# Kernel optimization log

Measured on AMD Instinct MI355X. Metric: run time of the kernel, lower is better.

Reference implementation:

```python
import jax, jax.numpy as jnp
import numpy as np

K = 7      # kernel size per spatial dim (kernel=[7,7])
PAD = 3    # padding per side ('same' for stride 1)
COUT = 64  # output width of the per-patch linear func


def _unfold(x):
    """convPrep: pad + unfold into sliding-window patches.
    x: [B, H, W] -> patches [B, H, W, K*K] (im2col, zero 'constant' padding)."""
    p = jax.lax.conv_general_dilated_patches(
        x[:, None, :, :],                # [B, 1, H, W]
        filter_shape=(K, K),
        window_strides=(1, 1),
        padding=[(PAD, PAD), (PAD, PAD)])
    # p: [B, K*K, H, W] -> [B, H, W, K*K]
    return jnp.moveaxis(p, 1, -1)


def setup_inputs() -> dict:
    key = jax.random.key(0)
    k1, k2 = jax.random.split(key, 2)
    x = jax.random.normal(k1, (8, 384, 384), dtype=jnp.float32)
    W = jax.random.normal(k2, (K * K, COUT), dtype=jnp.float32) / np.sqrt(K * K).astype(np.float32)
    b = jnp.zeros((COUT,), dtype=jnp.float32)
    return {"x": x, "W": W, "b": b}


def reference(x, W, b):
    # convPrep (pad+unfold) -> func (linear per flattened patch) -> convPost (fold back)
    patches = _unfold(x)                               # [B, H, W, K*K]
    out = jnp.einsum('bhwk,kc->bhwc', patches, W) + b  # [B, H, W, COUT]
    return out
```

## Files before the change

### kernel.cpp

```cpp
#include <hip/hip_runtime.h>


#define HH 384
#define WWID 384
#define BB 8
#define COUTC 64
#define TPX 64
#define TILES_PER_ROW 6
#define NTILES (BB * HH * TILES_PER_ROW)
#define NBLOCKS 2048
#define TILES_PER_BLOCK (NTILES / NBLOCKS)

typedef __attribute__((ext_vector_type(8))) __bf16 bf16x8;
typedef __attribute__((ext_vector_type(4))) float f32x4;

__global__ __launch_bounds__(256)
void conv7_mfma(const float* __restrict__ xg, const float* __restrict__ wg,
                const float* __restrict__ bg, float* __restrict__ out)
{
    __shared__ __bf16 xt[10][72];
    const int tid  = threadIdx.x;
    const int lane = tid & 63;
    const int wv   = tid >> 6;
    const int lq   = lane >> 4;
    const int lr   = lane & 15;

    bf16x8 bfr[2][4];
#pragma unroll
    for (int ch = 0; ch < 2; ++ch)
#pragma unroll
        for (int g = 0; g < 4; ++g) {
            bf16x8 f;
#pragma unroll
            for (int j = 0; j < 8; ++j) {
                const int k = ch * 32 + lq * 8 + j;
                f[j] = (k < 49) ? (__bf16)wg[k * COUTC + g * 16 + lr] : (__bf16)0.f;
            }
            bfr[ch][g] = f;
        }
    float biasv[4];
#pragma unroll
    for (int g = 0; g < 4; ++g) biasv[g] = bg[g * 16 + lr];

    int aoffp[2][8];
#pragma unroll
    for (int ch = 0; ch < 2; ++ch)
#pragma unroll
        for (int j = 0; j < 8; ++j) {
            const int k  = ch * 32 + lq * 8 + j;
            const int ky = k / 7, kx = k - ky * 7;
            aoffp[ch][j] = ky * 72 + kx + wv * 16 + lr;
        }

    for (int i = tid; i < 3 * 72; i += 256)
        (&xt[0][0])[7 * 72 + i] = (__bf16)0.f;

    for (int it = 0; it < TILES_PER_BLOCK; ++it) {
        const int tile = blockIdx.x * TILES_PER_BLOCK + it;
        const int t  = tile % TILES_PER_ROW;
        const int rh = tile / TILES_PER_ROW;
        const int h  = rh % HH;
        const int b  = rh / HH;
        const int w0 = t * TPX;

        __syncthreads();
        for (int i = tid; i < 490; i += 256) {
            const int r  = i / 70;
            const int c  = i - r * 70;
            const int hs = h - 3 + r;
            const int ws = w0 - 3 + c;
            float v = 0.f;
            if (hs >= 0 && hs < HH && ws >= 0 && ws < WWID)
                v = xg[((size_t)b * HH + hs) * WWID + ws];
            xt[r][c] = (__bf16)v;
        }
        __syncthreads();

        bf16x8 af[2];
#pragma unroll
        for (int ch = 0; ch < 2; ++ch) {
            bf16x8 f;
#pragma unroll
            for (int j = 0; j < 8; ++j)
                f[j] = (&xt[0][0])[aoffp[ch][j]];
            af[ch] = f;
        }

        f32x4 acc[4];
#pragma unroll
        for (int g = 0; g < 4; ++g)
            acc[g] = (f32x4){biasv[g], biasv[g], biasv[g], biasv[g]};
#pragma unroll
        for (int ch = 0; ch < 2; ++ch)
#pragma unroll
            for (int g = 0; g < 4; ++g)
                acc[g] = __builtin_amdgcn_mfma_f32_16x16x32_bf16(
                    af[ch], bfr[ch][g], acc[g], 0, 0, 0);

        float* obase = out + (((size_t)b * HH + h) * WWID + w0 + wv * 16) * COUTC;
#pragma unroll
        for (int g = 0; g < 4; ++g)
#pragma unroll
            for (int rr = 0; rr < 4; ++rr)
                obase[(size_t)(lq * 4 + rr) * COUTC + g * 16 + lr] = acc[g][rr];
    }
}

extern "C" void kernel_launch(void* const* d_in, const int* in_sizes, int n_in,
                              void* d_out, int out_size, void* d_ws, size_t ws_size,
                              hipStream_t stream) {
    const float* x = (const float*)d_in[0];
    const float* w = (const float*)d_in[1];
    const float* b = (const float*)d_in[2];
    float* out = (float*)d_out;
    (void)in_sizes; (void)n_in; (void)out_size; (void)d_ws; (void)ws_size;
    conv7_mfma<<<NBLOCKS, 256, 0, stream>>>(x, w, b, out);
}
```

Measured before the change: 330.5 us.

## Drop LDS staging; load patches from global and swap MFMA operands for vector stores

Removes the shared-memory tile and block-wide barriers, so each wave independently loads its 7x8 input window directly from global memory into registers, with a fast interior path and a clamped border path. The K dimension is re-laid out as ky*8+kx with zero padding so each lane's fragment is a contiguous row segment. MFMA operands are swapped (weights as A, input as B), which lets each lane write four contiguous output channels as a single float4 store instead of scalar strided stores. The cost is redundant global loads across lanes and waves, which now rely on cache hits.

```diff
diff --git a/kernel.cpp b/kernel.cpp
--- a/kernel.cpp
+++ b/kernel.cpp
@@ -2,30 +2,31 @@
 
 
 #define HH 384
-#define WWID 384
+#define WW 384
 #define BB 8
-#define COUTC 64
-#define TPX 64
-#define TILES_PER_ROW 6
-#define NTILES (BB * HH * TILES_PER_ROW)
+#define CC 64
+#define TPW 16
+#define TROW (WW / TPW)
+#define NTILES (BB * HH * TROW)
 #define NBLOCKS 2048
-#define TILES_PER_BLOCK (NTILES / NBLOCKS)
+#define WPB 4
+#define NWAVES (NBLOCKS * WPB)
+#define TPWAVE (NTILES / NWAVES)
 
 typedef __attribute__((ext_vector_type(8))) __bf16 bf16x8;
 typedef __attribute__((ext_vector_type(4))) float f32x4;
 
 __global__ __launch_bounds__(256)
-void conv7_mfma(const float* __restrict__ xg, const float* __restrict__ wg,
-                const float* __restrict__ bg, float* __restrict__ out)
+void conv7_mfma_nolds(const float* __restrict__ xg, const float* __restrict__ wg,
+                      const float* __restrict__ bg, float* __restrict__ out)
 {
-    __shared__ __bf16 xt[10][72];
     const int tid  = threadIdx.x;
     const int lane = tid & 63;
     const int wv   = tid >> 6;
     const int lq   = lane >> 4;
     const int lr   = lane & 15;
 
-    bf16x8 bfr[2][4];
+    bf16x8 wfr[2][4];
 #pragma unroll
     for (int ch = 0; ch < 2; ++ch)
 #pragma unroll
@@ -33,76 +34,75 @@
             bf16x8 f;
 #pragma unroll
             for (int j = 0; j < 8; ++j) {
-                const int k = ch * 32 + lq * 8 + j;
-                f[j] = (k < 49) ? (__bf16)wg[k * COUTC + g * 16 + lr] : (__bf16)0.f;
+                const int ky = ch * 4 + lq;
+                const int kx = j;
+                f[j] = (ky < 7 && kx < 7) ? (__bf16)wg[(ky * 7 + kx) * CC + g * 16 + lr]
+                                          : (__bf16)0.f;
             }
-            bfr[ch][g] = f;
+            wfr[ch][g] = f;
         }
-    float biasv[4];
+    f32x4 biasf[4];
 #pragma unroll
-    for (int g = 0; g < 4; ++g) biasv[g] = bg[g * 16 + lr];
+    for (int g = 0; g < 4; ++g)
+        biasf[g] = *(const f32x4*)(bg + g * 16 + lq * 4);
 
-    int aoffp[2][8];
-#pragma unroll
-    for (int ch = 0; ch < 2; ++ch)
-#pragma unroll
-        for (int j = 0; j < 8; ++j) {
-            const int k  = ch * 32 + lq * 8 + j;
-            const int ky = k / 7, kx = k - ky * 7;
-            aoffp[ch][j] = ky * 72 + kx + wv * 16 + lr;
-        }
+    const int gw = blockIdx.x * WPB + wv;
 
-    for (int i = tid; i < 3 * 72; i += 256)
-        (&xt[0][0])[7 * 72 + i] = (__bf16)0.f;
-
-    for (int it = 0; it < TILES_PER_BLOCK; ++it) {
-        const int tile = blockIdx.x * TILES_PER_BLOCK + it;
-        const int t  = tile % TILES_PER_ROW;
-        const int rh = tile / TILES_PER_ROW;
+    for (int it = 0; it < TPWAVE; ++it) {
+        const int tile = gw * TPWAVE + it;
+        const int tw = tile % TROW;
+        const int rh = tile / TROW;
         const int h  = rh % HH;
         const int b  = rh / HH;
-        const int w0 = t * TPX;
+        const int w0 = tw * TPW;
 
-        __syncthreads();
-        for (int i = tid; i < 490; i += 256) {
-            const int r  = i / 70;
-            const int c  = i - r * 70;
-            const int hs = h - 3 + r;
-            const int ws = w0 - 3 + c;
-            float v = 0.f;
-            if (hs >= 0 && hs < HH && ws >= 0 && ws < WWID)
-                v = xg[((size_t)b * HH + hs) * WWID + ws];
-            xt[r][c] = (__bf16)v;
-        }
-        __syncthreads();
-
-        bf16x8 af[2];
+        bf16x8 xf[2];
+        const bool interior = (h >= 3) & (h <= HH - 5) & (w0 != 0) & (w0 != WW - TPW);
+        if (interior) {
+            const float* p0 = xg + ((size_t)b * HH + (h - 3)) * WW + (w0 - 3 + lr);
 #pragma unroll
-        for (int ch = 0; ch < 2; ++ch) {
-            bf16x8 f;
+            for (int ch = 0; ch < 2; ++ch) {
+                float v[8];
+                __builtin_memcpy(v, p0 + (size_t)(ch * 4 + lq) * WW, 32);
+                bf16x8 f;
 #pragma unroll
-            for (int j = 0; j < 8; ++j)
-                f[j] = (&xt[0][0])[aoffp[ch][j]];
-            af[ch] = f;
+                for (int j = 0; j < 8; ++j) f[j] = (__bf16)v[j];
+                xf[ch] = f;
+            }
+        } else {
+#pragma unroll
+            for (int ch = 0; ch < 2; ++ch) {
+                const int r  = h - 3 + ch * 4 + lq;
+                const int rc = r < 0 ? 0 : (r > HH - 1 ? HH - 1 : r);
+                const bool rok = (r >= 0) & (r < HH);
+                const float* prow = xg + ((size_t)b * HH + rc) * WW;
+                bf16x8 f;
+#pragma unroll
+                for (int j = 0; j < 8; ++j) {
+                    const int c  = w0 - 3 + lr + j;
+                    const int cc = c < 0 ? 0 : (c > WW - 1 ? WW - 1 : c);
+                    float v = prow[cc];
+                    v = (rok & (c >= 0) & (c < WW)) ? v : 0.f;
+                    f[j] = (__bf16)v;
+                }
+                xf[ch] = f;
+            }
         }
 
         f32x4 acc[4];
 #pragma unroll
-        for (int g = 0; g < 4; ++g)
-            acc[g] = (f32x4){biasv[g], biasv[g], biasv[g], biasv[g]};
+        for (int g = 0; g < 4; ++g) acc[g] = biasf[g];
 #pragma unroll
         for (int ch = 0; ch < 2; ++ch)
 #pragma unroll
             for (int g = 0; g < 4; ++g)
                 acc[g] = __builtin_amdgcn_mfma_f32_16x16x32_bf16(
-                    af[ch], bfr[ch][g], acc[g], 0, 0, 0);
+                    wfr[ch][g], xf[ch], acc[g], 0, 0, 0);
 
-        float* obase = out + (((size_t)b * HH + h) * WWID + w0 + wv * 16) * COUTC;
+        float* op = out + (((size_t)b * HH + h) * WW + w0 + lr) * CC + lq * 4;
 #pragma unroll
         for (int g = 0; g < 4; ++g)
-#pragma unroll
-            for (int rr = 0; rr < 4; ++rr)
-                obase[(size_t)(lq * 4 + rr) * COUTC + g * 16 + lr] = acc[g][rr];
+            *(f32x4*)(op + g * 16) = acc[g];
     }
 }
 
@@ -114,5 +114,5 @@
     const float* b = (const float*)d_in[2];
     float* out = (float*)d_out;
     (void)in_sizes; (void)n_in; (void)out_size; (void)d_ws; (void)ws_size;
-    conv7_mfma<<<NBLOCKS, 256, 0, stream>>>(x, w, b, out);
+    conv7_mfma_nolds<<<NBLOCKS, 256, 0, stream>>>(x, w, b, out);
 }
```

Result: no change. 330.9 us (+0.1%).
